# Optimization experiments

Hardware: AMD Instinct MI355X
Metric: run time of the kernel (lower is better)

Reference implementation:

```python
import jax, jax.numpy as jnp
import numpy as np

N = 32768
D = 256
NUM_POS = 4
TEMPS = 2
ID_NUM = N // TEMPS // NUM_POS  # 4096


def setup_inputs() -> dict:
    key = jax.random.key(0)
    k1, _ = jax.random.split(key)
    inputs = jax.random.normal(k1, (N, D), dtype=jnp.float32)
    # two modality halves, each half = each id repeated NUM_POS times
    targets = (jnp.arange(N, dtype=jnp.int64) // NUM_POS) % ID_NUM
    return {"inputs": inputs, "targets": targets}


def reference(inputs, targets):
    eps = 1e-6
    num_pos, temps = NUM_POS, TEMPS
    n = inputs.shape[0]
    id_num = n // temps // num_pos

    # centers: per-id mean (original python loop over ids == segment mean)
    ones = jnp.ones((n,), inputs.dtype)
    counts = jax.ops.segment_sum(ones, targets, num_segments=id_num)  # [id_num]
    centers = jax.ops.segment_sum(inputs, targets, num_segments=id_num) / counts[:, None]  # [id_num, D]

    # pairwise euclidean distance centers -> inputs  [id_num, N]
    d2 = (jnp.sum(centers * centers, axis=1)[:, None]
          + jnp.sum(inputs * inputs, axis=1)[None, :]
          - 2.0 * centers @ inputs.T)
    dist = jnp.sqrt(jnp.clip(d2, 1e-12, None))

    # is_neg_c2i: id of each center vs every sample
    center_ids = targets[jnp.arange(id_num) * num_pos]  # [id_num]
    is_neg = center_ids[:, None] != targets[None, :]    # [id_num, N]

    # negative mining (masked, fixed-shape version of an[an>1e-6].view)
    an = jnp.where(is_neg, dist, 0.0)
    valid_neg = an > eps
    n_neg = jnp.sum(valid_neg, axis=1).astype(dist.dtype)           # = N - temps*num_pos
    d_neg = jnp.sum(jnp.where(valid_neg, an, 0.0), axis=1) / n_neg  # per-center mean neg dist
    hard = valid_neg & (an < d_neg[:, None])                        # hard negatives (closer than mean)
    hard_cnt = jnp.sum(hard, axis=1).astype(dist.dtype)
    row_an = jnp.sum(jnp.where(hard, an, 0.0), axis=1) / hard_cnt   # per-center hard-neg mean
    an_mean = jnp.mean(row_an)

    # positives: center to its own samples
    ap = jnp.where(is_neg, 0.0, dist)
    valid_pos = ap > eps
    ap_mean = jnp.sum(jnp.where(valid_pos, ap, 0.0)) / jnp.sum(valid_pos).astype(dist.dtype)

    return ap_mean / an_mean
```

## Files before the change

kernel.cpp:

```cpp
#include <hip/hip_runtime.h>
#include <hip/hip_bf16.h>

#define NS   32768
#define DD   256
#define NPOS 4
#define IDN  4096

#define QSCALE 15.9375f
#define QBIAS  (-158.875f)
#define QINV   0.0627451f

typedef __attribute__((ext_vector_type(8))) short short8;
typedef __attribute__((ext_vector_type(4))) float f32x4;

__device__ __forceinline__ unsigned short f2bf(float f) {
    unsigned int u = __builtin_bit_cast(unsigned int, f);
    unsigned int r = (u + 0x7FFFu + ((u >> 16) & 1u)) >> 16;
    return (unsigned short)r;
}

__device__ __forceinline__ void gload16(const void* g, void* lds) {
    __builtin_amdgcn_global_load_lds(
        (const __attribute__((address_space(1))) unsigned int*)g,
        (__attribute__((address_space(3))) unsigned int*)lds, 16, 0, 0);
}

__device__ __forceinline__ float qdequant(unsigned int q) {
    return fmaf((float)q, QINV, 10.0f);
}
__device__ __forceinline__ unsigned int qquant(float d) {
    float t = fmaf(d, QSCALE, QBIAS);
    t = fminf(255.0f, fmaxf(0.0f, t));
    return (unsigned int)t;
}


__global__ __launch_bounds__(256)
void prep_k(const float* __restrict__ in, unsigned short* __restrict__ Xb,
            float* __restrict__ x2, unsigned short* __restrict__ Cb,
            float* __restrict__ c2, float* __restrict__ possum,
            float* __restrict__ posdist) {
    const int r = blockIdx.x;
    const int d = threadIdx.x;
    const int lane = d & 63, wv = d >> 6;

    int rows[8];
    #pragma unroll
    for (int j = 0; j < 8; ++j)
        rows[j] = (j < 4) ? (4 * r + j) : (16384 + 4 * r + (j - 4));

    float v[8];
    #pragma unroll
    for (int j = 0; j < 8; ++j) v[j] = in[(size_t)rows[j] * DD + d];

    float c = (v[0] + v[1] + v[2] + v[3] + v[4] + v[5] + v[6] + v[7]) * 0.125f;
    Cb[(size_t)r * DD + d] = f2bf(c);
    #pragma unroll
    for (int j = 0; j < 8; ++j)
        Xb[(size_t)rows[j] * DD + d] = f2bf(v[j]);

    float part[17];
    #pragma unroll
    for (int j = 0; j < 8; ++j) { part[j] = v[j] * v[j]; part[8 + j] = c * v[j]; }
    part[16] = c * c;
    #pragma unroll
    for (int k = 0; k < 17; ++k)
        #pragma unroll
        for (int m = 1; m < 64; m <<= 1)
            part[k] += __shfl_xor(part[k], m, 64);

    __shared__ float red2[17][4];
    __shared__ float fin[17];
    __shared__ float pdsh[8];
    if (lane == 0)
        #pragma unroll
        for (int k = 0; k < 17; ++k) red2[k][wv] = part[k];
    __syncthreads();
    if (d < 17) fin[d] = red2[d][0] + red2[d][1] + red2[d][2] + red2[d][3];
    __syncthreads();

    if (d < 8) {
        x2[rows[d]] = fin[d];
        float d2 = fin[16] + fin[d] - 2.f * fin[8 + d];
        float dist = sqrtf(fmaxf(d2, 1e-12f));
        posdist[r * 8 + d] = dist;
        pdsh[d] = dist;
    }
    __syncthreads();
    if (d == 0) {
        c2[r] = fin[16];
        possum[r] = pdsh[0] + pdsh[1] + pdsh[2] + pdsh[3]
                  + pdsh[4] + pdsh[5] + pdsh[6] + pdsh[7];
    }
}

__global__ void dneg_k(const float* __restrict__ negsum_all,
                       const float* __restrict__ possum,
                       const float* __restrict__ posdist,
                       float* __restrict__ dnout,
                       float* __restrict__ pcs, float* __restrict__ pcc, int mode) {
    int r = blockIdx.x * 256 + threadIdx.x;
    if (r < IDN) {
        float dn = (negsum_all[r] - possum[r]) * (1.0f / 32760.0f);
        dnout[r] = mode ? dn : dn * dn;
        float s = 0.f, c = 0.f;
        #pragma unroll
        for (int j = 0; j < 8; ++j) {
            float d = posdist[r * 8 + j];
            if (mode) d = qdequant(qquant(d));
            if (d < dn) { s += d; c += 1.f; }
        }
        pcs[r] = s; pcc[r] = c;
    }
}


template <bool STORE>
__global__ __launch_bounds__(512, 2)
void mpass1_k(const unsigned short* __restrict__ Cb, const unsigned short* __restrict__ Xb,
              const float* __restrict__ c2, const float* __restrict__ x2,
              float* __restrict__ S, unsigned char* __restrict__ D2) {
    __shared__ unsigned short As[64 * 512];
    __shared__ unsigned short Bs[2 * 32 * 512];

    const int tid = threadIdx.x;
    const int l  = tid & 63;
    const int w  = tid >> 6;
    const int wr = w >> 2;
    const int wc = w & 3;
    const int lr = l & 15;
    const int lc = l >> 4;
    const int bid = blockIdx.x;
    const int ch = bid & 7;
    const int bm = bid >> 3;
    const int colbase = ch * 4096;

    const unsigned short* bj[4]; unsigned int bslot[4];
    #pragma unroll
    for (int j = 0; j < 4; ++j) {
        const int s = w * 4 + j;
        const int kk2s = s >> 4;
        const int cbs  = s & 15;
        bj[j] = Xb + (size_t)(colbase + cbs * 16 + lr) * DD + kk2s * 32 + lc * 8;
        bslot[j] = (unsigned)(kk2s * 16 + cbs) * 512;
    }

    {
        const unsigned short* asrc = Cb + (size_t)(bm * 128 + lr) * DD + w * 32 + lc * 8;
        #pragma unroll
        for (int rb = 0; rb < 8; ++rb)
            gload16(asrc + (size_t)rb * 16 * DD, &As[(w * 8 + rb) * 512]);
        #pragma unroll
        for (int j = 0; j < 4; ++j)
            gload16(bj[j], &Bs[bslot[j]]);
    }
    __syncthreads();

    const int gr0 = bm * 128 + wr * 64;
    float c2v[16];
    #pragma unroll
    for (int mf = 0; mf < 4; ++mf)
        #pragma unroll
        for (int r = 0; r < 4; ++r)
            c2v[mf * 4 + r] = c2[gr0 + mf * 16 + lc * 4 + r];

    float rs[16];
    #pragma unroll
    for (int i = 0; i < 16; ++i) rs[i] = 0.f;

    unsigned char* dbase = STORE ? (D2 + (size_t)bid * 524288 + (size_t)w * 1024 + l * 16)
                                 : nullptr;

    for (int step = 0; step < 16; ++step) {
        float x2v[4];
        #pragma unroll
        for (int nf = 0; nf < 4; ++nf)
            x2v[nf] = x2[colbase + step * 256 + wc * 64 + nf * 16 + lr];

        f32x4 acc[4][4];
        #pragma unroll
        for (int a = 0; a < 4; ++a)
            #pragma unroll
            for (int b = 0; b < 4; ++b) acc[a][b] = (f32x4){0.f, 0.f, 0.f, 0.f};

        #pragma unroll
        for (int ss = 0; ss < 4; ++ss) {
            const int g  = step * 4 + ss;
            const int gn = (g + 1) & 63;
            {
                const size_t go = (size_t)(gn >> 2) * (256 * DD) + (gn & 3) * 64;
                const unsigned int doff = (unsigned)(gn & 1) * 16384;
                #pragma unroll
                for (int j = 0; j < 4; ++j)
                    gload16(bj[j] + go, &Bs[doff + bslot[j]]);
            }
            const unsigned int boff = (unsigned)(g & 1) * 16384;
            #pragma unroll
            for (int kk2 = 0; kk2 < 2; ++kk2) {
                const int kkg = ss * 2 + kk2;
                short8 af[4], bf[4];
                #pragma unroll
                for (int mf = 0; mf < 4; ++mf)
                    af[mf] = *(const short8*)&As[((kkg * 8) + wr * 4 + mf) * 512 + l * 8];
                #pragma unroll
                for (int nf = 0; nf < 4; ++nf)
                    bf[nf] = *(const short8*)&Bs[boff + (kk2 * 16 + wc * 4 + nf) * 512 + l * 8];
                __builtin_amdgcn_s_setprio(1);
                #pragma unroll
                for (int mf = 0; mf < 4; ++mf)
                    #pragma unroll
                    for (int nf = 0; nf < 4; ++nf)
                        acc[mf][nf] = __builtin_amdgcn_mfma_f32_16x16x32_bf16(
                            af[mf], bf[nf], acc[mf][nf], 0, 0, 0);
                __builtin_amdgcn_s_setprio(0);
            }
            __syncthreads();
        }

        #pragma unroll
        for (int mf = 0; mf < 4; ++mf) {
            unsigned int pw[4];
            #pragma unroll
            for (int r = 0; r < 4; ++r) {
                const int i = mf * 4 + r;
                unsigned int b = 0;
                #pragma unroll
                for (int nf = 0; nf < 4; ++nf) {
                    float d2 = fmaf(-2.f, acc[mf][nf][r], c2v[i] + x2v[nf]);
                    float dist = __builtin_amdgcn_sqrtf(fmaxf(d2, 1e-12f));
                    rs[i] += dist;
                    if (STORE) b |= qquant(dist) << (8 * nf);
                }
                pw[r] = b;
            }
            if (STORE) {
                uint4 v; v.x = pw[0]; v.y = pw[1]; v.z = pw[2]; v.w = pw[3];
                *(uint4*)(dbase + (size_t)(step * 4 + mf) * 8192) = v;
            }
        }
    }

    #pragma unroll
    for (int i = 0; i < 16; ++i)
        #pragma unroll
        for (int m = 1; m < 16; m <<= 1)
            rs[i] += __shfl_xor(rs[i], m, 64);
    if (lr == 0) {
        #pragma unroll
        for (int mf = 0; mf < 4; ++mf)
            #pragma unroll
            for (int r = 0; r < 4; ++r)
                atomicAdd(&S[gr0 + mf * 16 + lc * 4 + r], rs[mf * 4 + r]);
    }
}

__global__ __launch_bounds__(512)
void hard_k(const unsigned char* __restrict__ D2, const float* __restrict__ dn,
            float* __restrict__ S, float* __restrict__ C) {
    const int tid = threadIdx.x;
    const int l  = tid & 63;
    const int w  = tid >> 6;
    const int wr = w >> 2;
    const int lc = l >> 4;
    const int lr = l & 15;
    const int bid2 = blockIdx.x;
    const int obid = bid2 >> 2;
    const int sub  = bid2 & 3;
    const int bm = obid >> 3;
    const int gr0 = bm * 128 + wr * 64;

    float dnv[16];
    #pragma unroll
    for (int mf = 0; mf < 4; ++mf)
        #pragma unroll
        for (int r = 0; r < 4; ++r)
            dnv[mf * 4 + r] = dn[gr0 + mf * 16 + lc * 4 + r];

    float rs[16], rc[16];
    #pragma unroll
    for (int i = 0; i < 16; ++i) { rs[i] = 0.f; rc[i] = 0.f; }

    const unsigned char* dbase = D2 + (size_t)obid * 524288 + (size_t)w * 1024 + l * 16;

    for (int s4 = 0; s4 < 4; ++s4) {
        const int step = sub * 4 + s4;
        #pragma unroll
        for (int mf = 0; mf < 4; ++mf) {
            uint4 v = *(const uint4*)(dbase + (size_t)(step * 4 + mf) * 8192);
            unsigned int pw[4] = {v.x, v.y, v.z, v.w};
            #pragma unroll
            for (int r = 0; r < 4; ++r) {
                const int i = mf * 4 + r;
                const float dni = dnv[i];
                #pragma unroll
                for (int nf = 0; nf < 4; ++nf) {
                    float d = qdequant((pw[r] >> (8 * nf)) & 0xFFu);
                    if (d < dni) { rs[i] += d; rc[i] += 1.f; }
                }
            }
        }
    }

    #pragma unroll
    for (int i = 0; i < 16; ++i)
        #pragma unroll
        for (int m = 1; m < 16; m <<= 1) {
            rs[i] += __shfl_xor(rs[i], m, 64);
            rc[i] += __shfl_xor(rc[i], m, 64);
        }
    if (lr == 0) {
        #pragma unroll
        for (int mf = 0; mf < 4; ++mf)
            #pragma unroll
            for (int r = 0; r < 4; ++r) {
                const int row = gr0 + mf * 16 + lc * 4 + r;
                atomicAdd(&S[row], rs[mf * 4 + r]);
                atomicAdd(&C[row], rc[mf * 4 + r]);
            }
    }
}

__global__ __launch_bounds__(512, 2)
void mpass2_k(const unsigned short* __restrict__ Cb, const unsigned short* __restrict__ Xb,
              const float* __restrict__ c2, const float* __restrict__ x2,
              const float* __restrict__ dneg2,
              float* __restrict__ S, float* __restrict__ C) {
    __shared__ unsigned short As[64 * 512];
    __shared__ unsigned short Bs[2 * 32 * 512];
    const int tid = threadIdx.x;
    const int l  = tid & 63;
    const int w  = tid >> 6;
    const int wr = w >> 2;
    const int wc = w & 3;
    const int lr = l & 15;
    const int lc = l >> 4;
    const int bid = blockIdx.x;
    const int ch = bid & 7;
    const int bm = bid >> 3;
    const int colbase = ch * 4096;
    const unsigned short* bj[4]; unsigned int bslot[4];
    #pragma unroll
    for (int j = 0; j < 4; ++j) {
        const int s = w * 4 + j;
        const int kk2s = s >> 4, cbs = s & 15;
        bj[j] = Xb + (size_t)(colbase + cbs * 16 + lr) * DD + kk2s * 32 + lc * 8;
        bslot[j] = (unsigned)(kk2s * 16 + cbs) * 512;
    }
    {
        const unsigned short* asrc = Cb + (size_t)(bm * 128 + lr) * DD + w * 32 + lc * 8;
        #pragma unroll
        for (int rb = 0; rb < 8; ++rb)
            gload16(asrc + (size_t)rb * 16 * DD, &As[(w * 8 + rb) * 512]);
        #pragma unroll
        for (int j = 0; j < 4; ++j) gload16(bj[j], &Bs[bslot[j]]);
    }
    __syncthreads();
    const int gr0 = bm * 128 + wr * 64;
    float c2v[16], dnv[16];
    #pragma unroll
    for (int mf = 0; mf < 4; ++mf)
        #pragma unroll
        for (int r = 0; r < 4; ++r) {
            const int row = gr0 + mf * 16 + lc * 4 + r;
            c2v[mf * 4 + r] = c2[row];
            dnv[mf * 4 + r] = dneg2[row];
        }
    float rs[16], rc[16];
    #pragma unroll
    for (int i = 0; i < 16; ++i) { rs[i] = 0.f; rc[i] = 0.f; }
    for (int step = 0; step < 16; ++step) {
        float x2v[4];
        #pragma unroll
        for (int nf = 0; nf < 4; ++nf)
            x2v[nf] = x2[colbase + step * 256 + wc * 64 + nf * 16 + lr];
        f32x4 acc[4][4];
        #pragma unroll
        for (int a = 0; a < 4; ++a)
            #pragma unroll
            for (int b = 0; b < 4; ++b) acc[a][b] = (f32x4){0.f, 0.f, 0.f, 0.f};
        #pragma unroll
        for (int ss = 0; ss < 4; ++ss) {
            const int g = step * 4 + ss, gn = (g + 1) & 63;
            {
                const size_t go = (size_t)(gn >> 2) * (256 * DD) + (gn & 3) * 64;
                const unsigned int doff = (unsigned)(gn & 1) * 16384;
                #pragma unroll
                for (int j = 0; j < 4; ++j) gload16(bj[j] + go, &Bs[doff + bslot[j]]);
            }
            const unsigned int boff = (unsigned)(g & 1) * 16384;
            #pragma unroll
            for (int kk2 = 0; kk2 < 2; ++kk2) {
                const int kkg = ss * 2 + kk2;
                short8 af[4], bf[4];
                #pragma unroll
                for (int mf = 0; mf < 4; ++mf)
                    af[mf] = *(const short8*)&As[((kkg * 8) + wr * 4 + mf) * 512 + l * 8];
                #pragma unroll
                for (int nf = 0; nf < 4; ++nf)
                    bf[nf] = *(const short8*)&Bs[boff + (kk2 * 16 + wc * 4 + nf) * 512 + l * 8];
                __builtin_amdgcn_s_setprio(1);
                #pragma unroll
                for (int mf = 0; mf < 4; ++mf)
                    #pragma unroll
                    for (int nf = 0; nf < 4; ++nf)
                        acc[mf][nf] = __builtin_amdgcn_mfma_f32_16x16x32_bf16(
                            af[mf], bf[nf], acc[mf][nf], 0, 0, 0);
                __builtin_amdgcn_s_setprio(0);
            }
            __syncthreads();
        }
        #pragma unroll
        for (int mf = 0; mf < 4; ++mf)
            #pragma unroll
            for (int nf = 0; nf < 4; ++nf)
                #pragma unroll
                for (int r = 0; r < 4; ++r) {
                    const int i = mf * 4 + r;
                    float d2 = fmaf(-2.f, acc[mf][nf][r], c2v[i] + x2v[nf]);
                    float d2c = fmaxf(d2, 1e-12f);
                    bool h = d2c < dnv[i];
                    rs[i] += h ? __builtin_amdgcn_sqrtf(d2c) : 0.f;
                    rc[i] += h ? 1.f : 0.f;
                }
    }
    #pragma unroll
    for (int i = 0; i < 16; ++i)
        #pragma unroll
        for (int m = 1; m < 16; m <<= 1) {
            rs[i] += __shfl_xor(rs[i], m, 64);
            rc[i] += __shfl_xor(rc[i], m, 64);
        }
    if (lr == 0) {
        #pragma unroll
        for (int mf = 0; mf < 4; ++mf)
            #pragma unroll
            for (int r = 0; r < 4; ++r) {
                const int row = gr0 + mf * 16 + lc * 4 + r;
                atomicAdd(&S[row], rs[mf * 4 + r]);
                atomicAdd(&C[row], rc[mf * 4 + r]);
            }
    }
}

__global__ void final_k(const float* __restrict__ hardsum,
                        const float* __restrict__ hardcnt,
                        const float* __restrict__ pcs, const float* __restrict__ pcc,
                        const float* __restrict__ possum, float* out) {
    float s_an = 0.f, s_ap = 0.f;
    for (int r = threadIdx.x; r < IDN; r += 256) {
        s_an += (hardsum[r] - pcs[r]) / fmaxf(hardcnt[r] - pcc[r], 1.0f);
        s_ap += possum[r];
    }
    #pragma unroll
    for (int m = 1; m < 64; m <<= 1) {
        s_an += __shfl_xor(s_an, m, 64);
        s_ap += __shfl_xor(s_ap, m, 64);
    }
    __shared__ float sb[8];
    int lane = threadIdx.x & 63, w = threadIdx.x >> 6;
    if (lane == 0) { sb[w] = s_an; sb[4 + w] = s_ap; }
    __syncthreads();
    if (threadIdx.x == 0) {
        float an = (sb[0] + sb[1] + sb[2] + sb[3]) / (float)IDN;
        float ap = (sb[4] + sb[5] + sb[6] + sb[7]) / (float)NS;
        out[0] = ap / an;
    }
}


extern "C" void kernel_launch(void* const* d_in, const int* in_sizes, int n_in,
                              void* d_out, int out_size, void* d_ws, size_t ws_size,
                              hipStream_t stream) {
    const float* inputs = (const float*)d_in[0];
    float* out = (float*)d_out;

    char* p = (char*)d_ws;
    unsigned short* Xb = (unsigned short*)p;  p += (size_t)NS * DD * 2;
    unsigned short* Cb = (unsigned short*)p;  p += (size_t)IDN * DD * 2;
    float* x2      = (float*)p;  p += (size_t)NS * 4;
    float* c2      = (float*)p;  p += (size_t)IDN * 4;
    float* dnbuf   = (float*)p;  p += (size_t)IDN * 4;
    float* possum  = (float*)p;  p += (size_t)IDN * 4;
    float* posdist = (float*)p;  p += (size_t)IDN * 8 * 4;
    float* pcs     = (float*)p;  p += (size_t)IDN * 4;
    float* pcc     = (float*)p;  p += (size_t)IDN * 4;
    char* zp = p;
    float* negsum  = (float*)p;  p += (size_t)IDN * 4;
    float* hardsum = (float*)p;  p += (size_t)IDN * 4;
    float* hardcnt = (float*)p;  p += (size_t)IDN * 4;
    p = (char*)(((size_t)p + 255) & ~(size_t)255);
    unsigned char* D2 = (unsigned char*)p;
    size_t required_big = (size_t)(p - (char*)d_ws) + (size_t)NS * IDN;

    const bool big = (ws_size >= required_big);

    hipMemsetAsync(zp, 0, (size_t)(3 * IDN * 4), stream);
    prep_k<<<IDN, 256, 0, stream>>>(inputs, Xb, x2, Cb, c2, possum, posdist);

    if (big) {
        mpass1_k<true><<<256, 512, 0, stream>>>(Cb, Xb, c2, x2, negsum, D2);
        dneg_k<<<IDN / 256, 256, 0, stream>>>(negsum, possum, posdist, dnbuf, pcs, pcc, 1);
        hard_k<<<1024, 512, 0, stream>>>(D2, dnbuf, hardsum, hardcnt);
    } else {
        mpass1_k<false><<<256, 512, 0, stream>>>(Cb, Xb, c2, x2, negsum, nullptr);
        dneg_k<<<IDN / 256, 256, 0, stream>>>(negsum, possum, posdist, dnbuf, pcs, pcc, 0);
        mpass2_k<<<256, 512, 0, stream>>>(Cb, Xb, c2, x2, dnbuf, hardsum, hardcnt);
    }
    final_k<<<1, 256, 0, stream>>>(hardsum, hardcnt, pcs, pcc, possum, out);
}
```

Baseline: 239.8 us.

## Stream B fragments into registers in distance kernel and fold dneg into hard/final

The distance GEMM kernel now uses 256-thread blocks covering 64 center rows each. Each wave loads its own 64-column B fragments directly from global memory into registers, prefetching two k-steps ahead. This removes the shared B double-buffer and the per-substep __syncthreads, at the cost of halving A reuse per block and reading X twice as often from cache or memory. The separate dneg_k launch is also dropped on the big-workspace path: the mean negative distance is recomputed inline in hard_k, and the positive-correction sums move into final_k.

```diff
diff --git a/kernel.cpp b/kernel.cpp
--- a/kernel.cpp
+++ b/kernel.cpp
@@ -98,16 +98,15 @@
                        const float* __restrict__ possum,
                        const float* __restrict__ posdist,
                        float* __restrict__ dnout,
-                       float* __restrict__ pcs, float* __restrict__ pcc, int mode) {
+                       float* __restrict__ pcs, float* __restrict__ pcc) {
     int r = blockIdx.x * 256 + threadIdx.x;
     if (r < IDN) {
         float dn = (negsum_all[r] - possum[r]) * (1.0f / 32760.0f);
-        dnout[r] = mode ? dn : dn * dn;
+        dnout[r] = dn * dn;
         float s = 0.f, c = 0.f;
         #pragma unroll
         for (int j = 0; j < 8; ++j) {
             float d = posdist[r * 8 + j];
-            if (mode) d = qdequant(qquant(d));
             if (d < dn) { s += d; c += 1.f; }
         }
         pcs[r] = s; pcc[r] = c;
@@ -116,47 +115,44 @@
 
 
 template <bool STORE>
-__global__ __launch_bounds__(512, 2)
+__global__ __launch_bounds__(256, 2)
 void mpass1_k(const unsigned short* __restrict__ Cb, const unsigned short* __restrict__ Xb,
               const float* __restrict__ c2, const float* __restrict__ x2,
               float* __restrict__ S, unsigned char* __restrict__ D2) {
-    __shared__ unsigned short As[64 * 512];
-    __shared__ unsigned short Bs[2 * 32 * 512];
+    __shared__ unsigned short As[32 * 512];
 
     const int tid = threadIdx.x;
     const int l  = tid & 63;
     const int w  = tid >> 6;
-    const int wr = w >> 2;
-    const int wc = w & 3;
     const int lr = l & 15;
     const int lc = l >> 4;
     const int bid = blockIdx.x;
     const int ch = bid & 7;
     const int bm = bid >> 3;
-    const int colbase = ch * 4096;
-
-    const unsigned short* bj[4]; unsigned int bslot[4];
-    #pragma unroll
-    for (int j = 0; j < 4; ++j) {
-        const int s = w * 4 + j;
-        const int kk2s = s >> 4;
-        const int cbs  = s & 15;
-        bj[j] = Xb + (size_t)(colbase + cbs * 16 + lr) * DD + kk2s * 32 + lc * 8;
-        bslot[j] = (unsigned)(kk2s * 16 + cbs) * 512;
-    }
+    const int colw0 = ch * 4096 + w * 64;
 
     {
-        const unsigned short* asrc = Cb + (size_t)(bm * 128 + lr) * DD + w * 32 + lc * 8;
-        #pragma unroll
-        for (int rb = 0; rb < 8; ++rb)
-            gload16(asrc + (size_t)rb * 16 * DD, &As[(w * 8 + rb) * 512]);
-        #pragma unroll
-        for (int j = 0; j < 4; ++j)
-            gload16(bj[j], &Bs[bslot[j]]);
-    }
+        const unsigned short* asrc = Cb + (size_t)(bm * 64 + lr) * DD + lc * 8;
+        #pragma unroll
+        for (int s2 = 0; s2 < 2; ++s2) {
+            const int kk = w * 2 + s2;
+            #pragma unroll
+            for (int rb = 0; rb < 4; ++rb)
+                gload16(asrc + (size_t)(rb * 16) * DD + kk * 32, &As[(kk * 4 + rb) * 512]);
+        }
+    }
+
+    const unsigned short* bbase = Xb + (size_t)(colw0 + lr) * DD + lc * 8;
+    short8 bR[2][4];
+    #pragma unroll
+    for (int s = 0; s < 2; ++s)
+        #pragma unroll
+        for (int nf = 0; nf < 4; ++nf)
+            bR[s][nf] = *(const short8*)(bbase + (size_t)(nf * 16) * DD + s * 32);
+
     __syncthreads();
 
-    const int gr0 = bm * 128 + wr * 64;
+    const int gr0 = bm * 64;
     float c2v[16];
     #pragma unroll
     for (int mf = 0; mf < 4; ++mf)
@@ -168,14 +164,18 @@
     #pragma unroll
     for (int i = 0; i < 16; ++i) rs[i] = 0.f;
 
-    unsigned char* dbase = STORE ? (D2 + (size_t)bid * 524288 + (size_t)w * 1024 + l * 16)
+    unsigned char* dbase = STORE ? (D2 + (size_t)bid * 262144 + (size_t)w * 1024 + l * 16)
                                  : nullptr;
 
     for (int step = 0; step < 16; ++step) {
+        const unsigned short* bnext = (step == 15)
+            ? (Xb + (size_t)(colw0 + lr) * DD + lc * 8)
+            : (bbase + (size_t)256 * DD);
+
         float x2v[4];
         #pragma unroll
         for (int nf = 0; nf < 4; ++nf)
-            x2v[nf] = x2[colbase + step * 256 + wc * 64 + nf * 16 + lr];
+            x2v[nf] = x2[ch * 4096 + step * 256 + w * 64 + nf * 16 + lr];
 
         f32x4 acc[4][4];
         #pragma unroll
@@ -184,37 +184,28 @@
             for (int b = 0; b < 4; ++b) acc[a][b] = (f32x4){0.f, 0.f, 0.f, 0.f};
 
         #pragma unroll
-        for (int ss = 0; ss < 4; ++ss) {
-            const int g  = step * 4 + ss;
-            const int gn = (g + 1) & 63;
+        for (int kk = 0; kk < 8; ++kk) {
+            const int s = kk & 1;
+            short8 af[4];
+            #pragma unroll
+            for (int mf = 0; mf < 4; ++mf)
+                af[mf] = *(const short8*)&As[((kk * 4) + mf) * 512 + l * 8];
+            __builtin_amdgcn_s_setprio(1);
+            #pragma unroll
+            for (int mf = 0; mf < 4; ++mf)
+                #pragma unroll
+                for (int nf = 0; nf < 4; ++nf)
+                    acc[mf][nf] = __builtin_amdgcn_mfma_f32_16x16x32_bf16(
+                        af[mf], bR[s][nf], acc[mf][nf], 0, 0, 0);
+            __builtin_amdgcn_s_setprio(0);
             {
-                const size_t go = (size_t)(gn >> 2) * (256 * DD) + (gn & 3) * 64;
-                const unsigned int doff = (unsigned)(gn & 1) * 16384;
-                #pragma unroll
-                for (int j = 0; j < 4; ++j)
-                    gload16(bj[j] + go, &Bs[doff + bslot[j]]);
-            }
-            const unsigned int boff = (unsigned)(g & 1) * 16384;
-            #pragma unroll
-            for (int kk2 = 0; kk2 < 2; ++kk2) {
-                const int kkg = ss * 2 + kk2;
-                short8 af[4], bf[4];
-                #pragma unroll
-                for (int mf = 0; mf < 4; ++mf)
-                    af[mf] = *(const short8*)&As[((kkg * 8) + wr * 4 + mf) * 512 + l * 8];
+                const int kn = kk + 2;
+                const unsigned short* sb = (kn < 8) ? bbase : bnext;
+                const int kidx = kn & 7;
                 #pragma unroll
                 for (int nf = 0; nf < 4; ++nf)
-                    bf[nf] = *(const short8*)&Bs[boff + (kk2 * 16 + wc * 4 + nf) * 512 + l * 8];
-                __builtin_amdgcn_s_setprio(1);
-                #pragma unroll
-                for (int mf = 0; mf < 4; ++mf)
-                    #pragma unroll
-                    for (int nf = 0; nf < 4; ++nf)
-                        acc[mf][nf] = __builtin_amdgcn_mfma_f32_16x16x32_bf16(
-                            af[mf], bf[nf], acc[mf][nf], 0, 0, 0);
-                __builtin_amdgcn_s_setprio(0);
-            }
-            __syncthreads();
+                    bR[s][nf] = *(const short8*)(sb + (size_t)(nf * 16) * DD + kidx * 32);
+            }
         }
 
         #pragma unroll
@@ -235,9 +226,11 @@
             }
             if (STORE) {
                 uint4 v; v.x = pw[0]; v.y = pw[1]; v.z = pw[2]; v.w = pw[3];
-                *(uint4*)(dbase + (size_t)(step * 4 + mf) * 8192) = v;
-            }
-        }
+                *(uint4*)(dbase + (size_t)(step * 4 + mf) * 4096) = v;
+            }
+        }
+
+        bbase = bnext;
     }
 
     #pragma unroll
@@ -254,39 +247,41 @@
     }
 }
 
-__global__ __launch_bounds__(512)
-void hard_k(const unsigned char* __restrict__ D2, const float* __restrict__ dn,
+__global__ __launch_bounds__(256)
+void hard_k(const unsigned char* __restrict__ D2,
+            const float* __restrict__ negsum, const float* __restrict__ possum,
             float* __restrict__ S, float* __restrict__ C) {
     const int tid = threadIdx.x;
     const int l  = tid & 63;
     const int w  = tid >> 6;
-    const int wr = w >> 2;
     const int lc = l >> 4;
     const int lr = l & 15;
     const int bid2 = blockIdx.x;
-    const int obid = bid2 >> 2;
-    const int sub  = bid2 & 3;
+    const int obid = bid2 >> 1;
+    const int half = bid2 & 1;
     const int bm = obid >> 3;
-    const int gr0 = bm * 128 + wr * 64;
+    const int gr0 = bm * 64;
 
     float dnv[16];
     #pragma unroll
     for (int mf = 0; mf < 4; ++mf)
         #pragma unroll
-        for (int r = 0; r < 4; ++r)
-            dnv[mf * 4 + r] = dn[gr0 + mf * 16 + lc * 4 + r];
+        for (int r = 0; r < 4; ++r) {
+            const int row = gr0 + mf * 16 + lc * 4 + r;
+            dnv[mf * 4 + r] = (negsum[row] - possum[row]) * (1.0f / 32760.0f);
+        }
 
     float rs[16], rc[16];
     #pragma unroll
     for (int i = 0; i < 16; ++i) { rs[i] = 0.f; rc[i] = 0.f; }
 
-    const unsigned char* dbase = D2 + (size_t)obid * 524288 + (size_t)w * 1024 + l * 16;
-
-    for (int s4 = 0; s4 < 4; ++s4) {
-        const int step = sub * 4 + s4;
+    const unsigned char* dbase = D2 + (size_t)obid * 262144 + (size_t)w * 1024 + l * 16;
+
+    for (int s8 = 0; s8 < 8; ++s8) {
+        const int step = half * 8 + s8;
         #pragma unroll
         for (int mf = 0; mf < 4; ++mf) {
-            uint4 v = *(const uint4*)(dbase + (size_t)(step * 4 + mf) * 8192);
+            uint4 v = *(const uint4*)(dbase + (size_t)(step * 4 + mf) * 4096);
             unsigned int pw[4] = {v.x, v.y, v.z, v.w};
             #pragma unroll
             for (int r = 0; r < 4; ++r) {
@@ -444,11 +439,20 @@
 
 __global__ void final_k(const float* __restrict__ hardsum,
                         const float* __restrict__ hardcnt,
-                        const float* __restrict__ pcs, const float* __restrict__ pcc,
-                        const float* __restrict__ possum, float* out) {
+                        const float* __restrict__ negsum,
+                        const float* __restrict__ possum,
+                        const float* __restrict__ posdist, float* out, int mode) {
     float s_an = 0.f, s_ap = 0.f;
     for (int r = threadIdx.x; r < IDN; r += 256) {
-        s_an += (hardsum[r] - pcs[r]) / fmaxf(hardcnt[r] - pcc[r], 1.0f);
+        float dn = (negsum[r] - possum[r]) * (1.0f / 32760.0f);
+        float s = 0.f, c = 0.f;
+        #pragma unroll
+        for (int j = 0; j < 8; ++j) {
+            float d = posdist[r * 8 + j];
+            if (mode) d = qdequant(qquant(d));
+            if (d < dn) { s += d; c += 1.f; }
+        }
+        s_an += (hardsum[r] - s) / fmaxf(hardcnt[r] - c, 1.0f);
         s_ap += possum[r];
     }
     #pragma unroll
@@ -498,13 +502,13 @@
     prep_k<<<IDN, 256, 0, stream>>>(inputs, Xb, x2, Cb, c2, possum, posdist);
 
     if (big) {
-        mpass1_k<true><<<256, 512, 0, stream>>>(Cb, Xb, c2, x2, negsum, D2);
-        dneg_k<<<IDN / 256, 256, 0, stream>>>(negsum, possum, posdist, dnbuf, pcs, pcc, 1);
-        hard_k<<<1024, 512, 0, stream>>>(D2, dnbuf, hardsum, hardcnt);
+        mpass1_k<true><<<512, 256, 0, stream>>>(Cb, Xb, c2, x2, negsum, D2);
+        hard_k<<<1024, 256, 0, stream>>>(D2, negsum, possum, hardsum, hardcnt);
+        final_k<<<1, 256, 0, stream>>>(hardsum, hardcnt, negsum, possum, posdist, out, 1);
     } else {
-        mpass1_k<false><<<256, 512, 0, stream>>>(Cb, Xb, c2, x2, negsum, nullptr);
-        dneg_k<<<IDN / 256, 256, 0, stream>>>(negsum, possum, posdist, dnbuf, pcs, pcc, 0);
+        mpass1_k<false><<<512, 256, 0, stream>>>(Cb, Xb, c2, x2, negsum, nullptr);
+        dneg_k<<<IDN / 256, 256, 0, stream>>>(negsum, possum, posdist, dnbuf, pcs, pcc);
         mpass2_k<<<256, 512, 0, stream>>>(Cb, Xb, c2, x2, dnbuf, hardsum, hardcnt);
-    }
-    final_k<<<1, 256, 0, stream>>>(hardsum, hardcnt, pcs, pcc, possum, out);
-}
+        final_k<<<1, 256, 0, stream>>>(hardsum, hardcnt, negsum, possum, posdist, out, 0);
+    }
+}
```

Result: faster. 226.2 us (-5.7%).
